# Kernel tuning notes

Measured on AMD Instinct MI355X. Metric: run time of the kernel, lower is better.

## Reference

```python
import jax, jax.numpy as jnp
import numpy as np

L = 3          # num encoder layers
H = 128        # hidden_dim
NH = 8         # num_heads
HD = H // NH   # head_dim
FF = H * 4     # ff inner dim (after GLU)
B, N = 32, 512
NUM_BINS = 50


def _linear_params(key, fan_in, fan_out):
    kw, kb = jax.random.split(key)
    lim = 1.0 / np.sqrt(fan_in)
    W = jax.random.uniform(kw, (fan_in, fan_out), jnp.float32, -lim, lim)
    b = jax.random.uniform(kb, (fan_out,), jnp.float32, -lim, lim)
    return W, b


def setup_inputs() -> dict:
    key = jax.random.key(0)
    ks = jax.random.split(key, 16)
    x = jax.random.normal(ks[0], (B, N, H), jnp.float32)
    distance_matrix = jax.random.uniform(ks[1], (B, N, N), jnp.float32)
    mask = jax.random.randint(ks[2], (B, N), 0, 2).astype(bool)

    def stack_linear(k, fan_in, fan_out):
        Ws, bs = [], []
        for l in range(L):
            W, b = _linear_params(jax.random.fold_in(k, l), fan_in, fan_out)
            Ws.append(W); bs.append(b)
        return jnp.stack(Ws), jnp.stack(bs)

    Wq, bq = stack_linear(ks[3], H, H)
    Wk, bk = stack_linear(ks[4], H, H)
    Wv, bv = stack_linear(ks[5], H, H)
    Wo, bo = stack_linear(ks[6], H, H)
    dist_emb = jax.random.normal(ks[7], (L, NUM_BINS, NH), jnp.float32)
    attn_bias = jnp.zeros((L, NH, 1, 1), jnp.float32)
    g1 = jnp.ones((L, H), jnp.float32); b1 = jnp.zeros((L, H), jnp.float32)
    g2 = jnp.ones((L, H), jnp.float32); b2 = jnp.zeros((L, H), jnp.float32)
    Wf1, bf1 = stack_linear(ks[8], H, 2 * FF)
    Wf2, bf2 = stack_linear(ks[9], FF, H)
    return dict(x=x, distance_matrix=distance_matrix, mask=mask,
                Wq=Wq, bq=bq, Wk=Wk, bk=bk, Wv=Wv, bv=bv, Wo=Wo, bo=bo,
                dist_emb=dist_emb, attn_bias=attn_bias,
                g1=g1, b1=b1, g2=g2, b2=b2,
                Wf1=Wf1, bf1=bf1, Wf2=Wf2, bf2=bf2)


def _layernorm(x, g, b, eps=1e-5):
    mu = jnp.mean(x, axis=-1, keepdims=True)
    var = jnp.var(x, axis=-1, keepdims=True)
    return (x - mu) * jax.lax.rsqrt(var + eps) * g + b


def _attention(h, bins, key_mask, Wq, bq, Wk, bk, Wv, bv, Wo, bo, dist_emb, attn_bias):
    # h: [B,N,H]; bins: [B,N,N] int; key_mask: [B,N] bool (True = masked)
    Bsz, Nn, _ = h.shape
    Q = (h @ Wq + bq).reshape(Bsz, Nn, NH, HD)
    K = (h @ Wk + bk).reshape(Bsz, Nn, NH, HD)
    V = (h @ Wv + bv).reshape(Bsz, Nn, NH, HD)
    scores = jnp.einsum('bqhd,bkhd->bhqk', Q, K) / np.sqrt(HD)
    bias = jnp.transpose(dist_emb[bins], (0, 3, 1, 2))  # [B,NH,N,N]
    scores = scores + bias + attn_bias[None]
    scores = jnp.where(key_mask[:, None, None, :], -1e9, scores)
    attn = jax.nn.softmax(scores, axis=-1)
    out = jnp.einsum('bhqk,bkhd->bqhd', attn, V).reshape(Bsz, Nn, H)
    return out @ Wo + bo


def reference(x, distance_matrix, mask, Wq, bq, Wk, bk, Wv, bv, Wo, bo,
              dist_emb, attn_bias, g1, b1, g2, b2, Wf1, bf1, Wf2, bf2):
    bins = jnp.clip((distance_matrix * 10.0).astype(jnp.int32), 0, NUM_BINS - 1)
    h = x
    for l in range(L):
        # pre-LN attention block
        a = _attention(_layernorm(h, g1[l], b1[l]), bins, mask,
                       Wq[l], bq[l], Wk[l], bk[l], Wv[l], bv[l], Wo[l], bo[l],
                       dist_emb[l], attn_bias[l])
        h = h + a
        # pre-LN GLU feed-forward
        u = _layernorm(h, g2[l], b2[l]) @ Wf1[l] + bf1[l]  # [B,N,2*FF]
        ua, ub = jnp.split(u, 2, axis=-1)
        h = h + (ua * jax.nn.sigmoid(ub)) @ Wf2[l] + bf2[l]
    return h
```

## Files before the change

kernel.cpp:

```cpp
#include <hip/hip_runtime.h>
#include <stdint.h>

#define Bq 32
#define Nq 512
#define Hq 128
#define NHq 8
#define HDq 16
#define Mq (Bq * Nq)

typedef unsigned short u16;
typedef __attribute__((ext_vector_type(8))) short short8;
typedef __attribute__((ext_vector_type(8))) _Float16 half8;
typedef __attribute__((ext_vector_type(2))) __fp16 fp16x2;
typedef __attribute__((ext_vector_type(4))) float f32x4;

__device__ __forceinline__ float bf2f(u16 v) {
    return __uint_as_float(((unsigned int)v) << 16);
}
__device__ __forceinline__ float ldin(const void* p, long idx, int bf) {
    if (bf) return bf2f(((const u16*)p)[idx]);
    return ((const float*)p)[idx];
}
__device__ __forceinline__ u16 f2bf(float v) {
    unsigned int u = __float_as_uint(v);
    return (u16)((u + 0x7FFFu + ((u >> 16) & 1u)) >> 16);
}
__device__ __forceinline__ u16 f2h(float v) {
    _Float16 h = (_Float16)v;
    return *(u16*)&h;
}
__device__ __forceinline__ unsigned pk2h(float a, float b) {
    fp16x2 c = __builtin_amdgcn_cvt_pkrtz(a, b);
    return *(unsigned*)&c;
}

__global__ void prep_kernel(const void* xraw, const void* de, const void* ab,
                            const void* mraw, int* flag, float* deo, float* abo,
                            unsigned* mbits, int n,
                            u16* __restrict__ kidxg, int* __restrict__ nkt,
                            unsigned* __restrict__ tmask) {
    __shared__ int cnt, orA, orB, orC, orD;
    __shared__ unsigned smb[512];
    int tid = threadIdx.x;
    if (tid == 0) { cnt = 0; orA = 0; orB = 0; orC = 0; orD = 0; }
    __syncthreads();
    const u16* u = (const u16*)xraw;
    int good = 0;
    for (int i = tid; i < 1024; i += 256) {
        u16 v = u[i];
        int e = (v >> 7) & 0xFF;
        if (v == 0 || (e >= 90 && e <= 141)) good++;
    }
    atomicAdd(&cnt, good);
    const uint4* p4 = (const uint4*)mraw;
    unsigned a = 0, b = 0, c = 0, d = 0;
    for (int i = tid; i < n / 16; i += 256) {
        uint4 w = p4[i];
        unsigned all = w.x | w.y | w.z | w.w;
        a |= all & 0xFEFEFEFEu;
        b |= all & 0x0000FF00u;
        c |= all & 0xFFFFFF00u;
        d |= w.y | w.w;
    }
    if (a) atomicOr(&orA, 1);
    if (b) atomicOr(&orB, 1);
    if (c) atomicOr(&orC, 1);
    if (d) atomicOr(&orD, 1);
    __syncthreads();
    int bf = (cnt >= 900);
    if (tid == 0) *flag = bf;
    int mode;
    if (orA) mode = orB ? 3 : 4;
    else if (orC) mode = 0;
    else mode = orD ? 1 : 2;
    for (int i = tid; i < 1200; i += 256) deo[i] = ldin(de, i, bf);
    if (tid < 24) abo[tid] = ldin(ab, tid, bf);
    const unsigned char* p = (const unsigned char*)mraw;
    for (int wI = tid; wI < n / 32; wI += 256) {
        unsigned word = 0;
        for (int j = 0; j < 32; ++j) {
            int i = wI * 32 + j;
            int v;
            switch (mode) {
                case 0: v = p[i]; break;
                case 1: v = ((const int*)p)[i]; break;
                case 2: v = (int)((const long long*)p)[i]; break;
                case 3: v = ((const u16*)p)[i] != 0; break;
                default: v = (((const float*)p)[i] != 0.0f); break;
            }
            if (v) word |= 1u << j;
        }
        mbits[wI] = word;
        smb[wI] = word;
    }
    __syncthreads();
    int lane = tid & 63;
    for (int bb = tid >> 6; bb < 32; bb += 4) {
        int pos_base = 0;
        for (int w = 0; w < 8; ++w) {
            unsigned lo = smb[bb * 16 + 2 * w], hi = smb[bb * 16 + 2 * w + 1];
            unsigned long long word = ((unsigned long long)hi << 32) | lo;
            unsigned long long un = ~word;
            int bit = (int)((un >> lane) & 1ull);
            unsigned long long before = un & ((1ull << lane) - 1ull);
            int pos = pos_base + __popcll(before);
            if (bit) kidxg[bb * 512 + pos] = (u16)(w * 64 + lane);
            pos_base += __popcll(un);
        }
        int nk = pos_base;
        int nkp = (nk + 31) & ~31;
        if (nkp == 0) nkp = 32;
        int nt = nkp >> 5;
        for (int j = nk + lane; j < nkp; j += 64) kidxg[bb * 512 + j] = 0;
        if (lane == 0) {
            nkt[bb] = nt;
            for (int t = 0; t < 16; ++t) tmask[bb * 16 + t] = 0;
            int rem = nk & 31;
            if (rem) tmask[bb * 16 + nt - 1] = 0xFFFFFFFFu << rem;
            if (nk == 0) tmask[bb * 16] = 0xFFFFFFFFu;
        }
    }
}

__global__ __launch_bounds__(256) void setup2_kernel(
    const void* __restrict__ dist, const u16* __restrict__ kidxg,
    const int* __restrict__ nktp, unsigned char* __restrict__ binsc,
    const void* x, float* __restrict__ h,
    const void* Wqr, const void* Wkr, const void* Wvr, const void* Wor,
    const void* Wf1r, const void* Wf2r,
    u16* qkvT, u16* oT, u16* f1T, u16* f2T, const int* flagp) {
    __shared__ u16 kl[512];
    __shared__ int ntS;
    __shared__ u16 Ts[32][33];
    int id = blockIdx.x;
    int tid = threadIdx.x;
    int bf = *flagp;
    if (id < 2048) {
        int b = id >> 6;
        int q0 = (id & 63) * 8;
        if (tid == 0) ntS = nktp[b];
        kl[tid] = kidxg[b * 512 + tid];
        kl[tid + 256] = kidxg[b * 512 + tid + 256];
        __syncthreads();
        int nkp = ntS * 32;
        for (int rq = 0; rq < 8; ++rq) {
            int q = q0 + rq;
            long rowoff = ((long)b * 512 + q) * 512;
            for (int j = tid; j < nkp; j += 256) {
                float d = ldin(dist, rowoff + kl[j], bf);
                int v = (int)(d * 10.0f);
                v = v < 0 ? 0 : (v > 49 ? 49 : v);
                binsc[((size_t)b * 512 + q) * 512 + j] = (unsigned char)(v << 2);
            }
        }
    } else if (id < 3072) {
        int i = (id - 2048) * 256 + tid;
        long base = (long)i * 8;
        if (bf) {
            uint4 w = ((const uint4*)x)[i];
            const u16* ws = (const u16*)&w;
            float o[8];
#pragma unroll
            for (int k = 0; k < 8; ++k) o[k] = bf2f(ws[k]);
            *(float4*)&h[base] = *(float4*)&o[0];
            *(float4*)&h[base + 4] = *(float4*)&o[4];
        } else {
            float4 a = ((const float4*)x)[2 * i];
            float4 b2v = ((const float4*)x)[2 * i + 1];
            *(float4*)&h[base] = a;
            *(float4*)&h[base + 4] = b2v;
        }
    } else {
        int bid = id - 3072;
        int l = bid >> 8, r = bid & 255;
        const void* src; u16* dst; long soff, doff; int Kd, Nd, t;
        if (r < 64) {
            int mat = r >> 4; t = r & 15; Kd = 128; Nd = 128;
            soff = (long)l * 16384;
            if (mat == 0)      { src = Wqr; dst = qkvT; doff = (long)l * 49152; }
            else if (mat == 1) { src = Wkr; dst = qkvT; doff = (long)l * 49152 + 16384; }
            else if (mat == 2) { src = Wvr; dst = qkvT; doff = (long)l * 49152 + 32768; }
            else               { src = Wor; dst = oT;   doff = (long)l * 16384; }
        } else if (r < 192) {
            t = r - 64; Kd = 128; Nd = 1024;
            src = Wf1r; soff = (long)l * 131072; dst = f1T; doff = (long)l * 131072;
        } else {
            t = r - 192; Kd = 512; Nd = 128;
            src = Wf2r; soff = (long)l * 65536; dst = f2T; doff = (long)l * 65536;
        }
        int ntile = Nd >> 5;
        int tk = t / ntile, tn = t % ntile;
        int rr = tid >> 3, cc0 = (tid & 7) * 4;
#pragma unroll
        for (int i = 0; i < 4; ++i) {
            long idx = soff + (long)(tk * 32 + rr) * Nd + tn * 32 + cc0 + i;
            Ts[rr][cc0 + i] = f2bf(ldin(src, idx, bf));
        }
        __syncthreads();
#pragma unroll
        for (int i = 0; i < 4; ++i) {
            long idx = doff + (long)(tn * 32 + rr) * Kd + tk * 32 + cc0 + i;
            dst[idx] = Ts[cc0 + i][rr];
        }
    }
}

__global__ __launch_bounds__(256, 4) void qkv_mfma_kernel(
    const float* __restrict__ h, const u16* __restrict__ qkvT_l,
    const void* bqr, const void* bkr, const void* bvr, long bOff,
    const void* g1raw, const void* b1raw, long lnOff,
    u16* __restrict__ Qo, u16* __restrict__ Ko, u16* __restrict__ Vo,
    const int* flagp) {
    __shared__ __align__(16) u16 As[32][136];
    int tid = threadIdx.x;
    int m0 = blockIdx.x * 32;
    int bf = *flagp;
    {
        int row = tid >> 3, c0 = (tid & 7) * 16;
        const float* hp = h + (size_t)(m0 + row) * 128 + c0;
        float4 f0 = *(const float4*)(hp);
        float4 f1 = *(const float4*)(hp + 4);
        float4 f2 = *(const float4*)(hp + 8);
        float4 f3 = *(const float4*)(hp + 12);
        float vv[16] = {f0.x, f0.y, f0.z, f0.w, f1.x, f1.y, f1.z, f1.w,
                        f2.x, f2.y, f2.z, f2.w, f3.x, f3.y, f3.z, f3.w};
        float s = 0.f, s2 = 0.f;
#pragma unroll
        for (int k = 0; k < 16; ++k) { s += vv[k]; s2 += vv[k] * vv[k]; }
#pragma unroll
        for (int o = 1; o < 8; o <<= 1) {
            s += __shfl_xor(s, o);
            s2 += __shfl_xor(s2, o);
        }
        float mu = s * (1.0f / 128.0f);
        float var = fmaxf(s2 * (1.0f / 128.0f) - mu * mu, 0.0f);
        float rstd = rsqrtf(var + 1e-5f);
        u16 tmp[16];
#pragma unroll
        for (int k = 0; k < 16; ++k) {
            float g = ldin(g1raw, lnOff + c0 + k, bf);
            float b = ldin(b1raw, lnOff + c0 + k, bf);
            tmp[k] = f2bf((vv[k] - mu) * rstd * g + b);
        }
        *(uint4*)&As[row][c0]     = *(uint4*)&tmp[0];
        *(uint4*)&As[row][c0 + 8] = *(uint4*)&tmp[8];
    }
    __syncthreads();
    int wave = tid >> 6, lane = tid & 63;
    int q = lane >> 4, ln = lane & 15;
    int nb = wave * 32;
    f32x4 zero = {0.f, 0.f, 0.f, 0.f};
#pragma unroll
    for (int mat = 0; mat < 3; ++mat) {
        const u16* WT = qkvT_l + (size_t)mat * 16384;
        const void* braw = mat == 0 ? bqr : (mat == 1 ? bkr : bvr);
        u16* C = mat == 0 ? Qo : (mat == 1 ? Ko : Vo);
        float scale = mat == 0 ? 0.25f : 1.0f;
        short8 bfr[2][4];
#pragma unroll
        for (int t = 0; t < 2; ++t)
#pragma unroll
            for (int k4 = 0; k4 < 4; ++k4)
                bfr[t][k4] = *(const short8*)(WT + (size_t)(nb + t * 16 + ln) * 128
                                              + k4 * 32 + q * 8);
        f32x4 acc[2][2];
#pragma unroll
        for (int i = 0; i < 2; ++i)
#pragma unroll
            for (int j = 0; j < 2; ++j) acc[i][j] = zero;
#pragma unroll
        for (int k4 = 0; k4 < 4; ++k4) {
            short8 af0 = *(const short8*)&As[ln][k4 * 32 + q * 8];
            short8 af1 = *(const short8*)&As[16 + ln][k4 * 32 + q * 8];
#pragma unroll
            for (int t = 0; t < 2; ++t) {
                acc[0][t] = __builtin_amdgcn_mfma_f32_16x16x32_bf16(
                    af0, bfr[t][k4], acc[0][t], 0, 0, 0);
                acc[1][t] = __builtin_amdgcn_mfma_f32_16x16x32_bf16(
                    af1, bfr[t][k4], acc[1][t], 0, 0, 0);
            }
        }
#pragma unroll
        for (int t = 0; t < 2; ++t) {
            int n = nb + t * 16 + ln;
            float bias = ldin(braw, bOff + n, bf);
#pragma unroll
            for (int mi = 0; mi < 2; ++mi)
#pragma unroll
                for (int r = 0; r < 4; ++r) {
                    int m = m0 + mi * 16 + q * 4 + r;
                    C[(size_t)m * 128 + n] = f2h((acc[mi][t][r] + bias) * scale);
                }
        }
    }
}

__global__ __launch_bounds__(256, 3) void ffglu_kernel(
    const u16* __restrict__ att, const u16* __restrict__ oT_l,
    const void* __restrict__ bo, long boOff, float* __restrict__ h,
    const void* g2, const void* b2, long ln2Off,
    const u16* __restrict__ f1T_l, const void* __restrict__ bf1r, long bf1Off,
    const u16* __restrict__ f2T_l, const void* __restrict__ bf2r, long bf2Off,
    void* __restrict__ outp, const int* flagp,
    const u16* __restrict__ qkvTn,
    const void* bqr, const void* bkr, const void* bvr, long bOffN,
    const void* g1, const void* b1, long ln1OffN,
    u16* __restrict__ Qo, u16* __restrict__ Ko, u16* __restrict__ Vo) {
    __shared__ __align__(16) u16 As[32][136];
    __shared__ __align__(16) u16 vg[32][520];
    __shared__ float stats[32][4][2];
    int tid = threadIdx.x;
    int m0 = blockIdx.x * 32;
    int wave = tid >> 6, lane = tid & 63;
    int q = lane >> 4, ln = lane & 15;
    int nb = wave * 32;
    int bf = *flagp;
    f32x4 zero = {0.f, 0.f, 0.f, 0.f};

#pragma unroll
    for (int i = 0; i < 2; ++i) {
        int idx = tid + i * 256; int r = idx >> 4, c = (idx & 15) << 3;
        *(uint4*)&As[r][c] = *(const uint4*)(att + (size_t)(m0 + r) * 128 + c);
    }
    __syncthreads();
    f32x4 acc[2][2];
#pragma unroll
    for (int i = 0; i < 2; ++i)
#pragma unroll
        for (int j = 0; j < 2; ++j) acc[i][j] = zero;
    {
        short8 bfr[2][4];
#pragma unroll
        for (int t = 0; t < 2; ++t)
#pragma unroll
            for (int k4 = 0; k4 < 4; ++k4)
                bfr[t][k4] = *(const short8*)(oT_l + (size_t)(nb + t * 16 + ln) * 128
                                              + k4 * 32 + q * 8);
#pragma unroll
        for (int k4 = 0; k4 < 4; ++k4) {
            short8 af0 = *(const short8*)&As[ln][k4 * 32 + q * 8];
            short8 af1 = *(const short8*)&As[16 + ln][k4 * 32 + q * 8];
#pragma unroll
            for (int t = 0; t < 2; ++t) {
                acc[0][t] = __builtin_amdgcn_mfma_f32_16x16x32_bf16(
                    af0, bfr[t][k4], acc[0][t], 0, 0, 0);
                acc[1][t] = __builtin_amdgcn_mfma_f32_16x16x32_bf16(
                    af1, bfr[t][k4], acc[1][t], 0, 0, 0);
            }
        }
    }
    float h1[2][2][4];
    float srow[2][4], s2row[2][4];
#pragma unroll
    for (int mi = 0; mi < 2; ++mi)
#pragma unroll
        for (int r = 0; r < 4; ++r) { srow[mi][r] = 0.f; s2row[mi][r] = 0.f; }
#pragma unroll
    for (int t = 0; t < 2; ++t) {
        int n = nb + t * 16 + ln;
        float bias = ldin(bo, boOff + n, bf);
#pragma unroll
        for (int mi = 0; mi < 2; ++mi)
#pragma unroll
            for (int r = 0; r < 4; ++r) {
                float v = acc[mi][t][r] + bias +
                          h[(size_t)(m0 + mi * 16 + q * 4 + r) * 128 + n];
                h1[mi][t][r] = v;
                srow[mi][r] += v; s2row[mi][r] += v * v;
            }
    }
#pragma unroll
    for (int mi = 0; mi < 2; ++mi)
#pragma unroll
        for (int r = 0; r < 4; ++r)
#pragma unroll
            for (int o = 1; o < 16; o <<= 1) {
                srow[mi][r] += __shfl_xor(srow[mi][r], o);
                s2row[mi][r] += __shfl_xor(s2row[mi][r], o);
            }
    if (ln == 0) {
#pragma unroll
        for (int mi = 0; mi < 2; ++mi)
#pragma unroll
            for (int r = 0; r < 4; ++r) {
                stats[mi * 16 + q * 4 + r][wave][0] = srow[mi][r];
                stats[mi * 16 + q * 4 + r][wave][1] = s2row[mi][r];
            }
    }
    __syncthreads();
    float mu[2][4], rs[2][4];
#pragma unroll
    for (int mi = 0; mi < 2; ++mi)
#pragma unroll
        for (int r = 0; r < 4; ++r) {
            int row = mi * 16 + q * 4 + r;
            float s = (stats[row][0][0] + stats[row][1][0]) +
                      (stats[row][2][0] + stats[row][3][0]);
            float s2 = (stats[row][0][1] + stats[row][1][1]) +
                       (stats[row][2][1] + stats[row][3][1]);
            mu[mi][r] = s * (1.0f / 128.0f);
            float var = fmaxf(s2 * (1.0f / 128.0f) - mu[mi][r] * mu[mi][r], 0.0f);
            rs[mi][r] = rsqrtf(var + 1e-5f);
        }
#pragma unroll
    for (int t = 0; t < 2; ++t) {
        int n = nb + t * 16 + ln;
        float g = ldin(g2, ln2Off + n, bf), bb = ldin(b2, ln2Off + n, bf);
#pragma unroll
        for (int mi = 0; mi < 2; ++mi)
#pragma unroll
            for (int r = 0; r < 4; ++r)
                As[mi * 16 + q * 4 + r][n] =
                    f2bf((h1[mi][t][r] - mu[mi][r]) * rs[mi][r] * g + bb);
    }
    __syncthreads();
    int nb16 = wave * 16;
    for (int ch = 0; ch < 8; ++ch) {
        int arow = ch * 64 + nb16;
        short8 ba[4], bb8[4];
#pragma unroll
        for (int k4 = 0; k4 < 4; ++k4) {
            ba[k4]  = *(const short8*)(f1T_l + (size_t)(arow + ln) * 128
                                       + k4 * 32 + q * 8);
            bb8[k4] = *(const short8*)(f1T_l + (size_t)(512 + arow + ln) * 128
                                       + k4 * 32 + q * 8);
        }
        f32x4 aA[2] = {zero, zero}, aB[2] = {zero, zero};
#pragma unroll
        for (int k4 = 0; k4 < 4; ++k4) {
            short8 af0 = *(const short8*)&As[ln][k4 * 32 + q * 8];
            short8 af1 = *(const short8*)&As[16 + ln][k4 * 32 + q * 8];
            aA[0] = __builtin_amdgcn_mfma_f32_16x16x32_bf16(af0, ba[k4], aA[0], 0, 0, 0);
            aA[1] = __builtin_amdgcn_mfma_f32_16x16x32_bf16(af1, ba[k4], aA[1], 0, 0, 0);
            aB[0] = __builtin_amdgcn_mfma_f32_16x16x32_bf16(af0, bb8[k4], aB[0], 0, 0, 0);
            aB[1] = __builtin_amdgcn_mfma_f32_16x16x32_bf16(af1, bb8[k4], aB[1], 0, 0, 0);
        }
        int n = arow + ln;
        float bA = ldin(bf1r, bf1Off + n, bf);
        float bB = ldin(bf1r, bf1Off + 512 + n, bf);
#pragma unroll
        for (int mi = 0; mi < 2; ++mi)
#pragma unroll
            for (int r = 0; r < 4; ++r) {
                float ua = aA[mi][r] + bA, ub = aB[mi][r] + bB;
                vg[mi * 16 + q * 4 + r][n] = f2bf(ua / (1.0f + __expf(-ub)));
            }
    }
    __syncthreads();
    f32x4 accF[2][2];
#pragma unroll
    for (int i = 0; i < 2; ++i)
#pragma unroll
        for (int j = 0; j < 2; ++j) accF[i][j] = zero;
    for (int fc = 0; fc < 4; ++fc) {
        short8 bfr[2][4];
#pragma unroll
        for (int t = 0; t < 2; ++t)
#pragma unroll
            for (int k4 = 0; k4 < 4; ++k4)
                bfr[t][k4] = *(const short8*)(f2T_l + (size_t)(nb + t * 16 + ln) * 512
                                              + fc * 128 + k4 * 32 + q * 8);
#pragma unroll
        for (int k4 = 0; k4 < 4; ++k4) {
            short8 af0 = *(const short8*)&vg[ln][fc * 128 + k4 * 32 + q * 8];
            short8 af1 = *(const short8*)&vg[16 + ln][fc * 128 + k4 * 32 + q * 8];
#pragma unroll
            for (int t = 0; t < 2; ++t) {
                accF[0][t] = __builtin_amdgcn_mfma_f32_16x16x32_bf16(
                    af0, bfr[t][k4], accF[0][t], 0, 0, 0);
                accF[1][t] = __builtin_amdgcn_mfma_f32_16x16x32_bf16(
                    af1, bfr[t][k4], accF[1][t], 0, 0, 0);
            }
        }
    }
#pragma unroll
    for (int t = 0; t < 2; ++t) {
        int n = nb + t * 16 + ln;
        float bias = ldin(bf2r, bf2Off + n, bf);
#pragma unroll
        for (int mi = 0; mi < 2; ++mi)
#pragma unroll
            for (int r = 0; r < 4; ++r) {
                int m = m0 + mi * 16 + q * 4 + r;
                float v = accF[mi][t][r] + bias + h1[mi][t][r];
                h[(size_t)m * 128 + n] = v;
                h1[mi][t][r] = v;
                if (outp) {
                    if (bf) ((u16*)outp)[(size_t)m * 128 + n] = f2bf(v);
                    else ((float*)outp)[(size_t)m * 128 + n] = v;
                }
            }
    }
    if (!qkvTn) return;
#pragma unroll
    for (int mi = 0; mi < 2; ++mi)
#pragma unroll
        for (int r = 0; r < 4; ++r) { srow[mi][r] = 0.f; s2row[mi][r] = 0.f; }
#pragma unroll
    for (int t = 0; t < 2; ++t)
#pragma unroll
        for (int mi = 0; mi < 2; ++mi)
#pragma unroll
            for (int r = 0; r < 4; ++r) {
                float v = h1[mi][t][r];
                srow[mi][r] += v; s2row[mi][r] += v * v;
            }
#pragma unroll
    for (int mi = 0; mi < 2; ++mi)
#pragma unroll
        for (int r = 0; r < 4; ++r)
#pragma unroll
            for (int o = 1; o < 16; o <<= 1) {
                srow[mi][r] += __shfl_xor(srow[mi][r], o);
                s2row[mi][r] += __shfl_xor(s2row[mi][r], o);
            }
    if (ln == 0) {
#pragma unroll
        for (int mi = 0; mi < 2; ++mi)
#pragma unroll
            for (int r = 0; r < 4; ++r) {
                stats[mi * 16 + q * 4 + r][wave][0] = srow[mi][r];
                stats[mi * 16 + q * 4 + r][wave][1] = s2row[mi][r];
            }
    }
    __syncthreads();
#pragma unroll
    for (int mi = 0; mi < 2; ++mi)
#pragma unroll
        for (int r = 0; r < 4; ++r) {
            int row = mi * 16 + q * 4 + r;
            float s = (stats[row][0][0] + stats[row][1][0]) +
                      (stats[row][2][0] + stats[row][3][0]);
            float s2 = (stats[row][0][1] + stats[row][1][1]) +
                       (stats[row][2][1] + stats[row][3][1]);
            mu[mi][r] = s * (1.0f / 128.0f);
            float var = fmaxf(s2 * (1.0f / 128.0f) - mu[mi][r] * mu[mi][r], 0.0f);
            rs[mi][r] = rsqrtf(var + 1e-5f);
        }
#pragma unroll
    for (int t = 0; t < 2; ++t) {
        int n = nb + t * 16 + ln;
        float g = ldin(g1, ln1OffN + n, bf), bb = ldin(b1, ln1OffN + n, bf);
#pragma unroll
        for (int mi = 0; mi < 2; ++mi)
#pragma unroll
            for (int r = 0; r < 4; ++r)
                As[mi * 16 + q * 4 + r][n] =
                    f2bf((h1[mi][t][r] - mu[mi][r]) * rs[mi][r] * g + bb);
    }
    __syncthreads();
#pragma unroll
    for (int mat = 0; mat < 3; ++mat) {
        const u16* WT = qkvTn + (size_t)mat * 16384;
        const void* braw = mat == 0 ? bqr : (mat == 1 ? bkr : bvr);
        u16* C = mat == 0 ? Qo : (mat == 1 ? Ko : Vo);
        float scale = mat == 0 ? 0.25f : 1.0f;
        short8 bfr[2][4];
#pragma unroll
        for (int t = 0; t < 2; ++t)
#pragma unroll
            for (int k4 = 0; k4 < 4; ++k4)
                bfr[t][k4] = *(const short8*)(WT + (size_t)(nb + t * 16 + ln) * 128
                                              + k4 * 32 + q * 8);
        f32x4 aq[2][2];
#pragma unroll
        for (int i = 0; i < 2; ++i)
#pragma unroll
            for (int j = 0; j < 2; ++j) aq[i][j] = zero;
#pragma unroll
        for (int k4 = 0; k4 < 4; ++k4) {
            short8 af0 = *(const short8*)&As[ln][k4 * 32 + q * 8];
            short8 af1 = *(const short8*)&As[16 + ln][k4 * 32 + q * 8];
#pragma unroll
            for (int t = 0; t < 2; ++t) {
                aq[0][t] = __builtin_amdgcn_mfma_f32_16x16x32_bf16(
                    af0, bfr[t][k4], aq[0][t], 0, 0, 0);
                aq[1][t] = __builtin_amdgcn_mfma_f32_16x16x32_bf16(
                    af1, bfr[t][k4], aq[1][t], 0, 0, 0);
            }
        }
#pragma unroll
        for (int t = 0; t < 2; ++t) {
            int n = nb + t * 16 + ln;
            float bias = ldin(braw, bOffN + n, bf);
#pragma unroll
            for (int mi = 0; mi < 2; ++mi)
#pragma unroll
                for (int r = 0; r < 4; ++r) {
                    int m = m0 + mi * 16 + q * 4 + r;
                    C[(size_t)m * 128 + n] = f2h((aq[mi][t][r] + bias) * scale);
                }
        }
    }
}

__global__ __launch_bounds__(256, 4) void attn_kernel(
    const u16* __restrict__ Qh, const u16* __restrict__ Kh,
    const u16* __restrict__ Vh, const unsigned char* __restrict__ binsc,
    const u16* __restrict__ kidxg, const int* __restrict__ nktp,
    const unsigned* __restrict__ tmaskp, const float* __restrict__ deL,
    const float* __restrict__ abL, u16* __restrict__ out) {
    int id = blockIdx.x;
    int c = id & 7, t5 = id >> 3;
    int nh = t5 & 7;
    int pair = ((t5 >> 3) << 3) | c;
    int b = pair >> 2, qq = pair & 3;

    __shared__ __align__(16) u16 KsF[8192];
    __shared__ __align__(16) u16 VT[16 * 520];
    __shared__ __align__(16) u16 Pl[4 * 16 * 40];

    int tid = threadIdx.x;
    int nt = __builtin_amdgcn_readfirstlane(nktp[b]);
    int nkp = nt * 32;
    const u16* Kp = Kh + (size_t)(b * Nq) * Hq + nh * HDq;
    const u16* Vp = Vh + (size_t)(b * Nq) * Hq + nh * HDq;
    for (int r = tid; r < nkp; r += 256) {
        int row = kidxg[b * 512 + r];
        int kt = r >> 5, s = (r >> 4) & 1, lnr = r & 15;
        uint4 k0v = *(const uint4*)(Kp + (size_t)row * Hq);
        uint4 k1v = *(const uint4*)(Kp + (size_t)row * Hq + 8);
        *(uint4*)&KsF[kt * 512 + s * 256 + lnr * 8]       = k0v;
        *(uint4*)&KsF[kt * 512 + s * 256 + 128 + lnr * 8] = k1v;
        uint4 v0 = *(const uint4*)(Vp + (size_t)row * Hq);
        uint4 v1 = *(const uint4*)(Vp + (size_t)row * Hq + 8);
        u16 vv[16];
        *(uint4*)&vv[0] = v0; *(uint4*)&vv[8] = v1;
#pragma unroll
        for (int d = 0; d < 16; ++d) VT[d * 520 + r] = vv[d];
    }
    __syncthreads();

    int wave = tid >> 6, lane = tid & 63;
    int quad = lane >> 4, ln = lane & 15;
    int q0w = qq * 128 + wave * 32;

    float tblf = (lane < 50) ? deL[lane * NHq + nh] + abL[nh] : 0.0f;
    int tbli = __float_as_int(tblf);
    unsigned tl = tmaskp[b * 16 + nt - 1];

    half8 qf[2];
#pragma unroll
    for (int t = 0; t < 2; ++t) {
        uint4 qv = {0, 0, 0, 0};
        if (quad < 2)
            qv = *(const uint4*)(Qh + (size_t)(b * Nq + q0w + t * 16 + ln) * Hq
                                 + nh * HDq + quad * 8);
        qf[t] = *(half8*)&qv;
    }

    f32x4 zero = {0.f, 0.f, 0.f, 0.f};
    f32x4 acc[2] = {zero, zero};
    float zp[2] = {0.f, 0.f};
    _Float16* Pw = (_Float16*)&Pl[wave * 640];
    const _Float16* KsH = (const _Float16*)KsF;
    const _Float16* VTH = (const _Float16*)VT;
    const unsigned char* brow0 = binsc + ((size_t)b * 512 + (q0w + ln)) * 512;
    const unsigned char* brow1 = brow0 + (size_t)16 * 512;

    unsigned pb00 = *(const unsigned*)(brow0 + quad * 4);
    unsigned pb01 = *(const unsigned*)(brow0 + 16 + quad * 4);
    unsigned pb10 = *(const unsigned*)(brow1 + quad * 4);
    unsigned pb11 = *(const unsigned*)(brow1 + 16 + quad * 4);

    for (int kt = 0; kt < nt; ++kt) {
        int k0 = kt * 32;
        unsigned w = (kt == nt - 1) ? tl : 0u;
        unsigned cb00 = pb00, cb01 = pb01, cb10 = pb10, cb11 = pb11;
        if (kt < nt - 1) {
            pb00 = *(const unsigned*)(brow0 + k0 + 32 + quad * 4);
            pb01 = *(const unsigned*)(brow0 + k0 + 48 + quad * 4);
            pb10 = *(const unsigned*)(brow1 + k0 + 32 + quad * 4);
            pb11 = *(const unsigned*)(brow1 + k0 + 48 + quad * 4);
        }
        half8 vb = *(const half8*)(VTH + ln * 520 + k0 + quad * 8);
        half8 ka0 = {}, ka1 = {};
        if (quad < 2) {
            ka0 = *(const half8*)(KsH + kt * 512 + quad * 128 + ln * 8);
            ka1 = *(const half8*)(KsH + kt * 512 + 256 + quad * 128 + ln * 8);
        }
#pragma unroll
        for (int t = 0; t < 2; ++t) {
            unsigned bw0 = t == 0 ? cb00 : cb10;
            unsigned bw1 = t == 0 ? cb01 : cb11;
            f32x4 s0 = __builtin_amdgcn_mfma_f32_16x16x32_f16(ka0, qf[t], zero, 0, 0, 0);
            f32x4 s1 = __builtin_amdgcn_mfma_f32_16x16x32_f16(ka1, qf[t], zero, 0, 0, 0);
            float p[8];
#pragma unroll
            for (int r = 0; r < 4; ++r) {
                float bias = __int_as_float(__builtin_amdgcn_ds_bpermute(
                    (int)((bw0 >> (8 * r)) & 0xFFu), tbli));
                float sc = s0[r] + bias;
                bool m = (w >> (quad * 4 + r)) & 1u;
                p[r] = m ? 0.0f : __expf(sc);
            }
#pragma unroll
            for (int r = 0; r < 4; ++r) {
                float bias = __int_as_float(__builtin_amdgcn_ds_bpermute(
                    (int)((bw1 >> (8 * r)) & 0xFFu), tbli));
                float sc = s1[r] + bias;
                bool m = (w >> (16 + quad * 4 + r)) & 1u;
                p[4 + r] = m ? 0.0f : __expf(sc);
            }
            zp[t] += ((p[0] + p[1]) + (p[2] + p[3])) +
                     ((p[4] + p[5]) + (p[6] + p[7]));
            uint2 w0, w1;
            w0.x = pk2h(p[0], p[1]); w0.y = pk2h(p[2], p[3]);
            w1.x = pk2h(p[4], p[5]); w1.y = pk2h(p[6], p[7]);
            *(uint2*)(Pw + ln * 40 + quad * 4)      = w0;
            *(uint2*)(Pw + ln * 40 + 16 + quad * 4) = w1;
            half8 pa = *(const half8*)(Pw + ln * 40 + quad * 8);
            acc[t] = __builtin_amdgcn_mfma_f32_16x16x32_f16(pa, vb, acc[t], 0, 0, 0);
        }
    }
#pragma unroll
    for (int t = 0; t < 2; ++t) {
        zp[t] += __shfl_xor(zp[t], 16);
        zp[t] += __shfl_xor(zp[t], 32);
    }
#pragma unroll
    for (int t = 0; t < 2; ++t) {
#pragma unroll
        for (int r = 0; r < 4; ++r) {
            float zz = __shfl(zp[t], quad * 4 + r);
            float val = acc[t][r] / fmaxf(zz, 1e-35f);
            int qrow = q0w + t * 16 + quad * 4 + r;
            out[(size_t)(b * Nq + qrow) * Hq + nh * HDq + ln] = f2bf(val);
        }
    }
}

extern "C" void kernel_launch(void* const* d_in, const int* in_sizes, int n_in,
                              void* d_out, int out_size, void* d_ws, size_t ws_size,
                              hipStream_t stream) {
    const void* x  = d_in[0];
    const void* dist = d_in[1];
    const void* mask = d_in[2];
    const void* Wq = d_in[3];  const void* bq = d_in[4];
    const void* Wk = d_in[5];  const void* bk = d_in[6];
    const void* Wv = d_in[7];  const void* bv = d_in[8];
    const void* Wo = d_in[9];  const void* bo = d_in[10];
    const void* de = d_in[11]; const void* ab = d_in[12];
    const void* g1 = d_in[13]; const void* b1 = d_in[14];
    const void* g2 = d_in[15]; const void* b2 = d_in[16];
    const void* Wf1 = d_in[17]; const void* bf1 = d_in[18];
    const void* Wf2 = d_in[19]; const void* bf2 = d_in[20];

    char* ws = (char*)d_ws;
    const size_t OFF_DE   = 64;
    const size_t OFF_AB   = 5120;
    const size_t OFF_BINS = 8192;
    const size_t OFF_MSK  = OFF_BINS + 8388608;
    const size_t OFF_KIDX = OFF_MSK + 4096;
    const size_t OFF_NKT  = OFF_KIDX + 32768;
    const size_t OFF_TM   = OFF_NKT + 256;
    const size_t OFF_H    = OFF_TM + 4096;
    const size_t OFF_QKV  = OFF_H + 8388608;
    const size_t OFF_ATT  = OFF_QKV + 25165824;
    const size_t OFF_WT   = OFF_ATT + 4194304;
    const size_t NEEDED   = OFF_WT + 1572864;
    if (ws_size < NEEDED) return;

    int* flag = (int*)ws;
    float* deF = (float*)(ws + OFF_DE);
    float* abF = (float*)(ws + OFF_AB);
    unsigned char* binsc = (unsigned char*)(ws + OFF_BINS);
    unsigned* mbits = (unsigned*)(ws + OFF_MSK);
    u16* kidxg = (u16*)(ws + OFF_KIDX);
    int* nkt = (int*)(ws + OFF_NKT);
    unsigned* tmask = (unsigned*)(ws + OFF_TM);
    float* h = (float*)(ws + OFF_H);
    u16* Qh = (u16*)(ws + OFF_QKV);
    u16* Kh = Qh + 2097152;
    u16* Vh = Qh + 2 * 2097152;
    u16* att = (u16*)(ws + OFF_ATT);
    u16* qkvT = (u16*)(ws + OFF_WT);
    u16* oT  = qkvT + 147456;
    u16* f1T = oT + 49152;
    u16* f2T = f1T + 393216;

    prep_kernel<<<1, 256, 0, stream>>>(x, de, ab, mask, flag, deF, abF, mbits,
                                       Bq * Nq, kidxg, nkt, tmask);
    setup2_kernel<<<3840, 256, 0, stream>>>(dist, kidxg, nkt, binsc, x, h,
                                            Wq, Wk, Wv, Wo, Wf1, Wf2,
                                            qkvT, oT, f1T, f2T, flag);
    qkv_mfma_kernel<<<512, 256, 0, stream>>>(h, qkvT, bq, bk, bv, 0,
                                             g1, b1, 0, Qh, Kh, Vh, flag);
    for (int l = 0; l < 3; ++l) {
        attn_kernel<<<1024, 256, 0, stream>>>(Qh, Kh, Vh, binsc, kidxg, nkt, tmask,
                                              deF + (long)l * 400, abF + (long)l * 8, att);
        ffglu_kernel<<<512, 256, 0, stream>>>(
            att, oT + (size_t)l * 16384, bo, (long)l * Hq,
            h, g2, b2, (long)l * Hq,
            f1T + (size_t)l * 131072, bf1, (long)l * 1024,
            f2T + (size_t)l * 65536, bf2, (long)l * Hq,
            l == 2 ? d_out : nullptr, flag,
            l < 2 ? qkvT + (size_t)(l + 1) * 49152 : (const u16*)nullptr,
            bq, bk, bv, (long)(l + 1) * Hq,
            g1, b1, (long)(l + 1) * Hq,
            Qh, Kh, Vh);
    }
}
```

Baseline: 355.2 us.

## Use 8 waves per block in FF-GLU kernel, one 16-column tile each

New measurement: 431.0 us. 1.21x slower.

```diff
diff --git a/kernel.cpp b/kernel.cpp
--- a/kernel.cpp
+++ b/kernel.cpp
@@ -295,7 +295,7 @@
     }
 }
 
-__global__ __launch_bounds__(256, 3) void ffglu_kernel(
+__global__ __launch_bounds__(512, 4) void ffglu_kernel(
     const u16* __restrict__ att, const u16* __restrict__ oT_l,
     const void* __restrict__ bo, long boOff, float* __restrict__ h,
     const void* g2, const void* b2, long ln2Off,
@@ -308,65 +308,46 @@
     u16* __restrict__ Qo, u16* __restrict__ Ko, u16* __restrict__ Vo) {
     __shared__ __align__(16) u16 As[32][136];
     __shared__ __align__(16) u16 vg[32][520];
-    __shared__ float stats[32][4][2];
+    __shared__ float stats[32][8][2];
     int tid = threadIdx.x;
     int m0 = blockIdx.x * 32;
     int wave = tid >> 6, lane = tid & 63;
     int q = lane >> 4, ln = lane & 15;
-    int nb = wave * 32;
+    int nb = wave * 16;
+    int n = nb + ln;
     int bf = *flagp;
     f32x4 zero = {0.f, 0.f, 0.f, 0.f};
 
-#pragma unroll
-    for (int i = 0; i < 2; ++i) {
-        int idx = tid + i * 256; int r = idx >> 4, c = (idx & 15) << 3;
-        *(uint4*)&As[r][c] = *(const uint4*)(att + (size_t)(m0 + r) * 128 + c);
-    }
-    __syncthreads();
-    f32x4 acc[2][2];
-#pragma unroll
-    for (int i = 0; i < 2; ++i)
-#pragma unroll
-        for (int j = 0; j < 2; ++j) acc[i][j] = zero;
+    { int r = tid >> 4, c = (tid & 15) << 3;
+      *(uint4*)&As[r][c] = *(const uint4*)(att + (size_t)(m0 + r) * 128 + c); }
+    __syncthreads();
+    f32x4 acc[2] = {zero, zero};
     {
-        short8 bfr[2][4];
-#pragma unroll
-        for (int t = 0; t < 2; ++t)
-#pragma unroll
-            for (int k4 = 0; k4 < 4; ++k4)
-                bfr[t][k4] = *(const short8*)(oT_l + (size_t)(nb + t * 16 + ln) * 128
-                                              + k4 * 32 + q * 8);
+        short8 bfr[4];
+#pragma unroll
+        for (int k4 = 0; k4 < 4; ++k4)
+            bfr[k4] = *(const short8*)(oT_l + (size_t)(nb + ln) * 128
+                                       + k4 * 32 + q * 8);
 #pragma unroll
         for (int k4 = 0; k4 < 4; ++k4) {
             short8 af0 = *(const short8*)&As[ln][k4 * 32 + q * 8];
             short8 af1 = *(const short8*)&As[16 + ln][k4 * 32 + q * 8];
-#pragma unroll
-            for (int t = 0; t < 2; ++t) {
-                acc[0][t] = __builtin_amdgcn_mfma_f32_16x16x32_bf16(
-                    af0, bfr[t][k4], acc[0][t], 0, 0, 0);
-                acc[1][t] = __builtin_amdgcn_mfma_f32_16x16x32_bf16(
-                    af1, bfr[t][k4], acc[1][t], 0, 0, 0);
-            }
-        }
-    }
-    float h1[2][2][4];
+            acc[0] = __builtin_amdgcn_mfma_f32_16x16x32_bf16(af0, bfr[k4], acc[0], 0, 0, 0);
+            acc[1] = __builtin_amdgcn_mfma_f32_16x16x32_bf16(af1, bfr[k4], acc[1], 0, 0, 0);
+        }
+    }
+    float h1[2][4];
     float srow[2][4], s2row[2][4];
-#pragma unroll
-    for (int mi = 0; mi < 2; ++mi)
-#pragma unroll
-        for (int r = 0; r < 4; ++r) { srow[mi][r] = 0.f; s2row[mi][r] = 0.f; }
-#pragma unroll
-    for (int t = 0; t < 2; ++t) {
-        int n = nb + t * 16 + ln;
-        float bias = ldin(bo, boOff + n, bf);
+    {
+        float biasO = ldin(bo, boOff + n, bf);
 #pragma unroll
         for (int mi = 0; mi < 2; ++mi)
 #pragma unroll
             for (int r = 0; r < 4; ++r) {
-                float v = acc[mi][t][r] + bias +
+                float v = acc[mi][r] + biasO +
                           h[(size_t)(m0 + mi * 16 + q * 4 + r) * 128 + n];
-                h1[mi][t][r] = v;
-                srow[mi][r] += v; s2row[mi][r] += v * v;
+                h1[mi][r] = v;
+                srow[mi][r] = v; s2row[mi][r] = v * v;
             }
     }
 #pragma unroll
@@ -394,29 +375,27 @@
 #pragma unroll
         for (int r = 0; r < 4; ++r) {
             int row = mi * 16 + q * 4 + r;
-            float s = (stats[row][0][0] + stats[row][1][0]) +
-                      (stats[row][2][0] + stats[row][3][0]);
-            float s2 = (stats[row][0][1] + stats[row][1][1]) +
-                       (stats[row][2][1] + stats[row][3][1]);
+            float s = 0.f, s2 = 0.f;
+#pragma unroll
+            for (int wv = 0; wv < 8; ++wv) {
+                s += stats[row][wv][0]; s2 += stats[row][wv][1];
+            }
             mu[mi][r] = s * (1.0f / 128.0f);
             float var = fmaxf(s2 * (1.0f / 128.0f) - mu[mi][r] * mu[mi][r], 0.0f);
             rs[mi][r] = rsqrtf(var + 1e-5f);
         }
-#pragma unroll
-    for (int t = 0; t < 2; ++t) {
-        int n = nb + t * 16 + ln;
+    {
         float g = ldin(g2, ln2Off + n, bf), bb = ldin(b2, ln2Off + n, bf);
 #pragma unroll
         for (int mi = 0; mi < 2; ++mi)
 #pragma unroll
             for (int r = 0; r < 4; ++r)
                 As[mi * 16 + q * 4 + r][n] =
-                    f2bf((h1[mi][t][r] - mu[mi][r]) * rs[mi][r] * g + bb);
-    }
-    __syncthreads();
-    int nb16 = wave * 16;
-    for (int ch = 0; ch < 8; ++ch) {
-        int arow = ch * 64 + nb16;
+                    f2bf((h1[mi][r] - mu[mi][r]) * rs[mi][r] * g + bb);
+    }
+    __syncthreads();
+    for (int ch = 0; ch < 4; ++ch) {
+        int arow = ch * 128 + nb;
         short8 ba[4], bb8[4];
 #pragma unroll
         for (int k4 = 0; k4 < 4; ++k4) {
@@ -435,56 +414,43 @@
             aB[0] = __builtin_amdgcn_mfma_f32_16x16x32_bf16(af0, bb8[k4], aB[0], 0, 0, 0);
             aB[1] = __builtin_amdgcn_mfma_f32_16x16x32_bf16(af1, bb8[k4], aB[1], 0, 0, 0);
         }
-        int n = arow + ln;
-        float bA = ldin(bf1r, bf1Off + n, bf);
-        float bB = ldin(bf1r, bf1Off + 512 + n, bf);
+        int nc = arow + ln;
+        float bA = ldin(bf1r, bf1Off + nc, bf);
+        float bB = ldin(bf1r, bf1Off + 512 + nc, bf);
 #pragma unroll
         for (int mi = 0; mi < 2; ++mi)
 #pragma unroll
             for (int r = 0; r < 4; ++r) {
                 float ua = aA[mi][r] + bA, ub = aB[mi][r] + bB;
-                vg[mi * 16 + q * 4 + r][n] = f2bf(ua / (1.0f + __expf(-ub)));
-            }
-    }
-    __syncthreads();
-    f32x4 accF[2][2];
-#pragma unroll
-    for (int i = 0; i < 2; ++i)
-#pragma unroll
-        for (int j = 0; j < 2; ++j) accF[i][j] = zero;
+                vg[mi * 16 + q * 4 + r][nc] = f2bf(ua / (1.0f + __expf(-ub)));
+            }
+    }
+    __syncthreads();
+    f32x4 accF[2] = {zero, zero};
     for (int fc = 0; fc < 4; ++fc) {
-        short8 bfr[2][4];
-#pragma unroll
-        for (int t = 0; t < 2; ++t)
-#pragma unroll
-            for (int k4 = 0; k4 < 4; ++k4)
-                bfr[t][k4] = *(const short8*)(f2T_l + (size_t)(nb + t * 16 + ln) * 512
-                                              + fc * 128 + k4 * 32 + q * 8);
+        short8 bfr[4];
+#pragma unroll
+        for (int k4 = 0; k4 < 4; ++k4)
+            bfr[k4] = *(const short8*)(f2T_l + (size_t)(nb + ln) * 512
+                                       + fc * 128 + k4 * 32 + q * 8);
 #pragma unroll
         for (int k4 = 0; k4 < 4; ++k4) {
             short8 af0 = *(const short8*)&vg[ln][fc * 128 + k4 * 32 + q * 8];
             short8 af1 = *(const short8*)&vg[16 + ln][fc * 128 + k4 * 32 + q * 8];
-#pragma unroll
-            for (int t = 0; t < 2; ++t) {
-                accF[0][t] = __builtin_amdgcn_mfma_f32_16x16x32_bf16(
-                    af0, bfr[t][k4], accF[0][t], 0, 0, 0);
-                accF[1][t] = __builtin_amdgcn_mfma_f32_16x16x32_bf16(
-                    af1, bfr[t][k4], accF[1][t], 0, 0, 0);
-            }
-        }
-    }
-#pragma unroll
-    for (int t = 0; t < 2; ++t) {
-        int n = nb + t * 16 + ln;
-        float bias = ldin(bf2r, bf2Off + n, bf);
+            accF[0] = __builtin_amdgcn_mfma_f32_16x16x32_bf16(af0, bfr[k4], accF[0], 0, 0, 0);
+            accF[1] = __builtin_amdgcn_mfma_f32_16x16x32_bf16(af1, bfr[k4], accF[1], 0, 0, 0);
+        }
+    }
+    {
+        float biasF = ldin(bf2r, bf2Off + n, bf);
 #pragma unroll
         for (int mi = 0; mi < 2; ++mi)
 #pragma unroll
             for (int r = 0; r < 4; ++r) {
                 int m = m0 + mi * 16 + q * 4 + r;
-                float v = accF[mi][t][r] + bias + h1[mi][t][r];
+                float v = accF[mi][r] + biasF + h1[mi][r];
                 h[(size_t)m * 128 + n] = v;
-                h1[mi][t][r] = v;
+                h1[mi][r] = v;
                 if (outp) {
                     if (bf) ((u16*)outp)[(size_t)m * 128 + n] = f2bf(v);
                     else ((float*)outp)[(size_t)m * 128 + n] = v;
@@ -495,16 +461,10 @@
 #pragma unroll
     for (int mi = 0; mi < 2; ++mi)
 #pragma unroll
-        for (int r = 0; r < 4; ++r) { srow[mi][r] = 0.f; s2row[mi][r] = 0.f; }
-#pragma unroll
-    for (int t = 0; t < 2; ++t)
-#pragma unroll
-        for (int mi = 0; mi < 2; ++mi)
-#pragma unroll
-            for (int r = 0; r < 4; ++r) {
-                float v = h1[mi][t][r];
-                srow[mi][r] += v; s2row[mi][r] += v * v;
-            }
+        for (int r = 0; r < 4; ++r) {
+            srow[mi][r] = h1[mi][r];
+            s2row[mi][r] = h1[mi][r] * h1[mi][r];
+        }
 #pragma unroll
     for (int mi = 0; mi < 2; ++mi)
 #pragma unroll
@@ -529,24 +489,23 @@
 #pragma unroll
         for (int r = 0; r < 4; ++r) {
             int row = mi * 16 + q * 4 + r;
-            float s = (stats[row][0][0] + stats[row][1][0]) +
-                      (stats[row][2][0] + stats[row][3][0]);
-            float s2 = (stats[row][0][1] + stats[row][1][1]) +
-                       (stats[row][2][1] + stats[row][3][1]);
+            float s = 0.f, s2 = 0.f;
+#pragma unroll
+            for (int wv = 0; wv < 8; ++wv) {
+                s += stats[row][wv][0]; s2 += stats[row][wv][1];
+            }
             mu[mi][r] = s * (1.0f / 128.0f);
             float var = fmaxf(s2 * (1.0f / 128.0f) - mu[mi][r] * mu[mi][r], 0.0f);
             rs[mi][r] = rsqrtf(var + 1e-5f);
         }
-#pragma unroll
-    for (int t = 0; t < 2; ++t) {
-        int n = nb + t * 16 + ln;
+    {
         float g = ldin(g1, ln1OffN + n, bf), bb = ldin(b1, ln1OffN + n, bf);
 #pragma unroll
         for (int mi = 0; mi < 2; ++mi)
 #pragma unroll
             for (int r = 0; r < 4; ++r)
                 As[mi * 16 + q * 4 + r][n] =
-                    f2bf((h1[mi][t][r] - mu[mi][r]) * rs[mi][r] * g + bb);
+                    f2bf((h1[mi][r] - mu[mi][r]) * rs[mi][r] * g + bb);
     }
     __syncthreads();
 #pragma unroll
@@ -555,42 +514,27 @@
         const void* braw = mat == 0 ? bqr : (mat == 1 ? bkr : bvr);
         u16* C = mat == 0 ? Qo : (mat == 1 ? Ko : Vo);
         float scale = mat == 0 ? 0.25f : 1.0f;
-        short8 bfr[2][4];
-#pragma unroll
-        for (int t = 0; t < 2; ++t)
-#pragma unroll
-            for (int k4 = 0; k4 < 4; ++k4)
-                bfr[t][k4] = *(const short8*)(WT + (size_t)(nb + t * 16 + ln) * 128
-                                              + k4 * 32 + q * 8);
-        f32x4 aq[2][2];
-#pragma unroll
-        for (int i = 0; i < 2; ++i)
-#pragma unroll
-            for (int j = 0; j < 2; ++j) aq[i][j] = zero;
+        short8 bfr[4];
+#pragma unroll
+        for (int k4 = 0; k4 < 4; ++k4)
+            bfr[k4] = *(const short8*)(WT + (size_t)(nb + ln) * 128
+                                       + k4 * 32 + q * 8);
+        f32x4 aq[2] = {zero, zero};
 #pragma unroll
         for (int k4 = 0; k4 < 4; ++k4) {
             short8 af0 = *(const short8*)&As[ln][k4 * 32 + q * 8];
             short8 af1 = *(const short8*)&As[16 + ln][k4 * 32 + q * 8];
-#pragma unroll
-            for (int t = 0; t < 2; ++t) {
-                aq[0][t] = __builtin_amdgcn_mfma_f32_16x16x32_bf16(
-                    af0, bfr[t][k4], aq[0][t], 0, 0, 0);
-                aq[1][t] = __builtin_amdgcn_mfma_f32_16x16x32_bf16(
-                    af1, bfr[t][k4], aq[1][t], 0, 0, 0);
-            }
-        }
-#pragma unroll
-        for (int t = 0; t < 2; ++t) {
-            int n = nb + t * 16 + ln;
-            float bias = ldin(braw, bOffN + n, bf);
-#pragma unroll
-            for (int mi = 0; mi < 2; ++mi)
-#pragma unroll
-                for (int r = 0; r < 4; ++r) {
-                    int m = m0 + mi * 16 + q * 4 + r;
-                    C[(size_t)m * 128 + n] = f2h((aq[mi][t][r] + bias) * scale);
-                }
-        }
+            aq[0] = __builtin_amdgcn_mfma_f32_16x16x32_bf16(af0, bfr[k4], aq[0], 0, 0, 0);
+            aq[1] = __builtin_amdgcn_mfma_f32_16x16x32_bf16(af1, bfr[k4], aq[1], 0, 0, 0);
+        }
+        float bias = ldin(braw, bOffN + n, bf);
+#pragma unroll
+        for (int mi = 0; mi < 2; ++mi)
+#pragma unroll
+            for (int r = 0; r < 4; ++r) {
+                int m = m0 + mi * 16 + q * 4 + r;
+                C[(size_t)m * 128 + n] = f2h((aq[mi][r] + bias) * scale);
+            }
     }
 }
 
@@ -789,7 +733,7 @@
     for (int l = 0; l < 3; ++l) {
         attn_kernel<<<1024, 256, 0, stream>>>(Qh, Kh, Vh, binsc, kidxg, nkt, tmask,
                                               deF + (long)l * 400, abF + (long)l * 8, att);
-        ffglu_kernel<<<512, 256, 0, stream>>>(
+        ffglu_kernel<<<512, 512, 0, stream>>>(
             att, oT + (size_t)l * 16384, bo, (long)l * Hq,
             h, g2, b2, (long)l * Hq,
             f1T + (size_t)l * 131072, bf1, (long)l * 1024,
```
